# Performance work log

Hardware: AMD Instinct MI355X
Metric: run time of the kernel (lower is better)

## Reference

```python
import jax, jax.numpy as jnp
import numpy as np

M, IN, OUT = 8192, 4096, 4096
XOR_MASK = (1 << 3) | (1 << 7)  # 0x88: flips sign bit of each packed nibble


def _dequant_int4(weight_packed, weight_scales):
    """Decode packed int4 weights (offset-binary nibbles) to scaled float.

    weight_packed: [OUT, IN//2] int32, each byte holds two nibbles (v+8).
    Low nibble -> even input column, high nibble -> odd input column.
    """
    w = jnp.bitwise_xor(weight_packed, XOR_MASK)  # offset-binary -> two's complement nibbles
    low = jnp.bitwise_and(w, 0xF)
    high = jnp.bitwise_and(jnp.right_shift(w, 4), 0xF)
    low = jnp.where(low >= 8, low - 16, low)    # signed int4 in [-8, 7]
    high = jnp.where(high >= 8, high - 16, high)
    # interleave nibbles: [OUT, IN//2, 2] -> [OUT, IN]
    deq = jnp.stack([low, high], axis=-1).reshape(weight_packed.shape[0], -1)
    return deq.astype(weight_scales.dtype) * weight_scales[:, None]  # [OUT, IN]


def setup_inputs() -> dict:
    key = jax.random.key(0)
    k1, k2, k3, k4 = jax.random.split(key, 4)
    x = jax.random.normal(k1, (M, IN), dtype=jnp.float32)
    weight_packed = jax.random.randint(k2, (OUT, IN // 2), 0, 256, dtype=jnp.int32)
    weight_scales = jax.random.uniform(k3, (OUT,), dtype=jnp.float32) * 0.02 + 1e-3
    bias = jax.random.normal(k4, (OUT,), dtype=jnp.float32)
    return {"x": x, "weight_packed": weight_packed,
            "weight_scales": weight_scales, "bias": bias}


def reference(x, weight_packed, weight_scales, bias):
    # w4a16 forward: dequantize int4 weights per output row, then GEMM + bias.
    w = _dequant_int4(weight_packed, weight_scales)  # [OUT, IN]
    return jnp.dot(x, w.T) + bias  # [M, OUT]
```

## Files before the change

kernel.cpp:

```cpp
#include <hip/hip_runtime.h>
#include <cstdint>
#include <cstddef>

#define M_DIM 8192
#define K_DIM 4096
#define N_DIM 4096

typedef unsigned short u16;
typedef __bf16 bf16x8 __attribute__((ext_vector_type(8)));
typedef u16 u16x8 __attribute__((ext_vector_type(8)));
typedef float f32x4 __attribute__((ext_vector_type(4)));

__device__ __forceinline__ u16 f2bf_rne(float f) {
  uint32_t u = __builtin_bit_cast(uint32_t, f);
  return (u16)((u + 0x7FFFu + ((u >> 16) & 1u)) >> 16);
}
__device__ __forceinline__ u16 i2bf(int i) {
  return (u16)(__builtin_bit_cast(uint32_t, (float)i) >> 16);
}

#define XBLKS 16384
#define WBLKS 8192

__global__ __launch_bounds__(256) void prep(const float* __restrict__ x,
                                            const int* __restrict__ wp,
                                            u16* __restrict__ xb,
                                            u16* __restrict__ wb) {
  const int b = blockIdx.x;
  if (b < XBLKS) {
    size_t t = (size_t)b * 256 + threadIdx.x;
    const float4* xp = (const float4*)x;
    float4 a = xp[2 * t];
    float4 c = xp[2 * t + 1];
    u16x8 r;
    r[0] = f2bf_rne(a.x); r[1] = f2bf_rne(a.y); r[2] = f2bf_rne(a.z); r[3] = f2bf_rne(a.w);
    r[4] = f2bf_rne(c.x); r[5] = f2bf_rne(c.y); r[6] = f2bf_rne(c.z); r[7] = f2bf_rne(c.w);
    ((u16x8*)xb)[t] = r;
  } else {
    size_t t = (size_t)(b - XBLKS) * 256 + threadIdx.x;
    int4 p = ((const int4*)wp)[t];
    u16x8 r;
    int v;
    v = p.x ^ 0x88; r[0] = i2bf((v << 28) >> 28); r[1] = i2bf((v << 24) >> 28);
    v = p.y ^ 0x88; r[2] = i2bf((v << 28) >> 28); r[3] = i2bf((v << 24) >> 28);
    v = p.z ^ 0x88; r[4] = i2bf((v << 28) >> 28); r[5] = i2bf((v << 24) >> 28);
    v = p.w ^ 0x88; r[6] = i2bf((v << 28) >> 28); r[7] = i2bf((v << 24) >> 28);
    ((u16x8*)wb)[t] = r;
  }
}

__global__ __launch_bounds__(512, 2) void gemm_bt_w4a16(
    const u16* __restrict__ A,
    const u16* __restrict__ B,
    const float* __restrict__ scales,
    const float* __restrict__ bias,
    float* __restrict__ C) {
  __shared__ u16 sA[2][256 * 64];
  __shared__ u16 sB[2][256 * 64];

  const int tid = threadIdx.x;
  const int lane = tid & 63;
  const int wave = tid >> 6;
  const int m0 = blockIdx.y * 256;
  const int n0 = blockIdx.x * 256;
  const int wm = (wave >> 2) * 128;
  const int wn = (wave & 3) * 64;
  const int lrow = lane & 15;
  const int quad = lane >> 4;

  f32x4 acc[8][4] = {};

  const int srow = tid >> 3;
  const int schunk = ((tid & 7) ^ (srow & 7)) * 8;
  const u16* ga = A + (size_t)(m0 + srow) * K_DIM + schunk;
  const u16* gb = B + (size_t)(n0 + srow) * K_DIM + schunk;
  const int ldsoff = wave * 1024;

  auto stage = [&](int buf, int kb) {
#pragma unroll
    for (int r = 0; r < 4; ++r)
      __builtin_amdgcn_global_load_lds(
          (const __attribute__((address_space(1))) void*)(ga + (size_t)(r * 64) * K_DIM + kb),
          (__attribute__((address_space(3))) void*)((char*)sA[buf] + r * 8192 + ldsoff),
          16, 0, 0);
#pragma unroll
    for (int r = 0; r < 4; ++r)
      __builtin_amdgcn_global_load_lds(
          (const __attribute__((address_space(1))) void*)(gb + (size_t)(r * 64) * K_DIM + kb),
          (__attribute__((address_space(3))) void*)((char*)sB[buf] + r * 8192 + ldsoff),
          16, 0, 0);
  };

  auto compute = [&](int buf) {
    const u16* bA = sA[buf];
    const u16* bB = sB[buf];
#pragma unroll
    for (int s = 0; s < 2; ++s) {
      const int kc = ((s * 4 + quad) ^ (lrow & 7)) * 8;
      u16x8 af[8], bfr[4];
#pragma unroll
      for (int i = 0; i < 8; ++i)
        af[i] = *(const u16x8*)(bA + (wm + i * 16 + lrow) * 64 + kc);
#pragma unroll
      for (int j = 0; j < 4; ++j)
        bfr[j] = *(const u16x8*)(bB + (wn + j * 16 + lrow) * 64 + kc);
      __builtin_amdgcn_s_setprio(1);
#pragma unroll
      for (int i = 0; i < 8; ++i)
#pragma unroll
        for (int j = 0; j < 4; ++j)
          acc[i][j] = __builtin_amdgcn_mfma_f32_16x16x32_bf16(
              __builtin_bit_cast(bf16x8, af[i]),
              __builtin_bit_cast(bf16x8, bfr[j]), acc[i][j], 0, 0, 0);
      __builtin_amdgcn_s_setprio(0);
    }
  };

  stage(0, 0);
  __syncthreads();

#pragma unroll 1
  for (int it = 0; it < 32; ++it) {
    const int kb = it * 128;
    stage(1, kb + 64);
    compute(0);
    __syncthreads();
    if (it < 31) stage(0, kb + 128);
    compute(1);
    __syncthreads();
  }

#pragma unroll
  for (int j = 0; j < 4; ++j) {
    const int n = n0 + wn + j * 16 + lrow;
    const float sc = scales[n];
    const float bi = bias[n];
#pragma unroll
    for (int i = 0; i < 8; ++i) {
      const int m = m0 + wm + i * 16 + quad * 4;
      float* cp = &C[(size_t)m * N_DIM + n];
#pragma unroll
      for (int r = 0; r < 4; ++r)
        cp[(size_t)r * N_DIM] = acc[i][j][r] * sc + bi;
    }
  }
}

__global__ __launch_bounds__(256) void fallback_w4a16(
    const float* __restrict__ x, const int* __restrict__ wp,
    const float* __restrict__ scales, const float* __restrict__ bias,
    float* __restrict__ out) {
  const int n = blockIdx.x * 256 + threadIdx.x;
  const int m = blockIdx.y;
  const float* xr = x + (size_t)m * K_DIM;
  const int* wr = wp + (size_t)n * (K_DIM / 2);
  float acc = 0.f;
  for (int j = 0; j < K_DIM / 2; ++j) {
    int w = wr[j] ^ 0x88;
    float lo = (float)((w << 28) >> 28);
    float hi = (float)((w << 24) >> 28);
    acc += xr[2 * j] * lo + xr[2 * j + 1] * hi;
  }
  out[(size_t)m * N_DIM + n] = acc * scales[n] + bias[n];
}

extern "C" void kernel_launch(void* const* d_in, const int* in_sizes, int n_in,
                              void* d_out, int out_size, void* d_ws, size_t ws_size,
                              hipStream_t stream) {
  const float* x = (const float*)d_in[0];
  const int* wp = (const int*)d_in[1];
  const float* sc = (const float*)d_in[2];
  const float* bi = (const float*)d_in[3];
  float* out = (float*)d_out;

  const size_t xb_elems = (size_t)M_DIM * K_DIM;
  const size_t wb_elems = (size_t)N_DIM * K_DIM;
  const size_t need = (xb_elems + wb_elems) * sizeof(u16);

  if (ws_size >= need) {
    u16* xb = (u16*)d_ws;
    u16* wb = xb + xb_elems;
    prep<<<XBLKS + WBLKS, 256, 0, stream>>>(x, wp, xb, wb);
    gemm_bt_w4a16<<<dim3(N_DIM / 256, M_DIM / 256), 512, 0, stream>>>(xb, wb, sc, bi, out);
  } else {
    fallback_w4a16<<<dim3(N_DIM / 256, M_DIM), 256, 0, stream>>>(x, wp, sc, bi, out);
  }
}
```

Before: 476.2 us.

## Switch GEMM to 256x128 tiles with triple-buffered LDS pipeline and block swizzle

The bf16 GEMM tile shrinks from 256x256 to 256x128, so each of the eight waves now computes a 64x64 sub-tile. The LDS staging changes from a double buffer with two barriers per step to a three-stage ring that is prefetched two tiles ahead, using a single barrier and a partial vmcnt wait per K step. A 1D grid with an XOR-free block remap groups neighbouring tiles to improve L2 reuse. The aim is to hide global-load latency and cut barrier stalls, at the cost of lower arithmetic intensity per tile and more LDS per block.

```diff
diff --git a/kernel.cpp b/kernel.cpp
--- a/kernel.cpp
+++ b/kernel.cpp
@@ -5,6 +5,12 @@
 #define M_DIM 8192
 #define K_DIM 4096
 #define N_DIM 4096
+
+#define BM 256
+#define BN 128
+#define BK 64
+#define NBUF 3
+#define NT (K_DIM / BK)
 
 typedef unsigned short u16;
 typedef __bf16 bf16x8 __attribute__((ext_vector_type(8)));
@@ -55,20 +61,26 @@
     const float* __restrict__ scales,
     const float* __restrict__ bias,
     float* __restrict__ C) {
-  __shared__ u16 sA[2][256 * 64];
-  __shared__ u16 sB[2][256 * 64];
+  __shared__ u16 sA[NBUF][BM * BK];
+  __shared__ u16 sB[NBUF][BN * BK];
 
   const int tid = threadIdx.x;
   const int lane = tid & 63;
   const int wave = tid >> 6;
-  const int m0 = blockIdx.y * 256;
-  const int n0 = blockIdx.x * 256;
-  const int wm = (wave >> 2) * 128;
-  const int wn = (wave & 3) * 64;
+
+  const int flat = blockIdx.x;
+  const int swz = (flat & 7) * 128 + (flat >> 3);
+  const int bx = swz >> 5;
+  const int by = swz & 31;
+  const int m0 = by * BM;
+  const int n0 = bx * BN;
+
+  const int wm = (wave >> 1) * 64;
+  const int wn = (wave & 1) * 64;
   const int lrow = lane & 15;
   const int quad = lane >> 4;
 
-  f32x4 acc[8][4] = {};
+  f32x4 acc[4][4] = {};
 
   const int srow = tid >> 3;
   const int schunk = ((tid & 7) ^ (srow & 7)) * 8;
@@ -84,7 +96,7 @@
           (__attribute__((address_space(3))) void*)((char*)sA[buf] + r * 8192 + ldsoff),
           16, 0, 0);
 #pragma unroll
-    for (int r = 0; r < 4; ++r)
+    for (int r = 0; r < 2; ++r)
       __builtin_amdgcn_global_load_lds(
           (const __attribute__((address_space(1))) void*)(gb + (size_t)(r * 64) * K_DIM + kb),
           (__attribute__((address_space(3))) void*)((char*)sB[buf] + r * 8192 + ldsoff),
@@ -97,16 +109,16 @@
 #pragma unroll
     for (int s = 0; s < 2; ++s) {
       const int kc = ((s * 4 + quad) ^ (lrow & 7)) * 8;
-      u16x8 af[8], bfr[4];
-#pragma unroll
-      for (int i = 0; i < 8; ++i)
-        af[i] = *(const u16x8*)(bA + (wm + i * 16 + lrow) * 64 + kc);
+      u16x8 af[4], bfr[4];
+#pragma unroll
+      for (int i = 0; i < 4; ++i)
+        af[i] = *(const u16x8*)(bA + (wm + i * 16 + lrow) * BK + kc);
 #pragma unroll
       for (int j = 0; j < 4; ++j)
-        bfr[j] = *(const u16x8*)(bB + (wn + j * 16 + lrow) * 64 + kc);
+        bfr[j] = *(const u16x8*)(bB + (wn + j * 16 + lrow) * BK + kc);
       __builtin_amdgcn_s_setprio(1);
 #pragma unroll
-      for (int i = 0; i < 8; ++i)
+      for (int i = 0; i < 4; ++i)
 #pragma unroll
         for (int j = 0; j < 4; ++j)
           acc[i][j] = __builtin_amdgcn_mfma_f32_16x16x32_bf16(
@@ -117,18 +129,28 @@
   };
 
   stage(0, 0);
-  __syncthreads();
-
+  stage(1, BK);
+
+  int cur = 0;
 #pragma unroll 1
-  for (int it = 0; it < 32; ++it) {
-    const int kb = it * 128;
-    stage(1, kb + 64);
-    compute(0);
-    __syncthreads();
-    if (it < 31) stage(0, kb + 128);
-    compute(1);
-    __syncthreads();
-  }
+  for (int t = 0; t < NT - 1; ++t) {
+    asm volatile("s_waitcnt vmcnt(6)" ::: "memory");
+    __builtin_amdgcn_s_barrier();
+    __builtin_amdgcn_sched_barrier(0);
+
+    if (t + 2 < NT) {
+      int pre = cur + 2;
+      if (pre >= NBUF) pre -= NBUF;
+      stage(pre, (t + 2) * BK);
+    }
+    compute(cur);
+    cur = (cur == NBUF - 1) ? 0 : cur + 1;
+  }
+
+  asm volatile("s_waitcnt vmcnt(0)" ::: "memory");
+  __builtin_amdgcn_s_barrier();
+  __builtin_amdgcn_sched_barrier(0);
+  compute(cur);
 
 #pragma unroll
   for (int j = 0; j < 4; ++j) {
@@ -136,7 +158,7 @@
     const float sc = scales[n];
     const float bi = bias[n];
 #pragma unroll
-    for (int i = 0; i < 8; ++i) {
+    for (int i = 0; i < 4; ++i) {
       const int m = m0 + wm + i * 16 + quad * 4;
       float* cp = &C[(size_t)m * N_DIM + n];
 #pragma unroll
@@ -181,7 +203,7 @@
     u16* xb = (u16*)d_ws;
     u16* wb = xb + xb_elems;
     prep<<<XBLKS + WBLKS, 256, 0, stream>>>(x, wp, xb, wb);
-    gemm_bt_w4a16<<<dim3(N_DIM / 256, M_DIM / 256), 512, 0, stream>>>(xb, wb, sc, bi, out);
+    gemm_bt_w4a16<<<dim3((N_DIM / BN) * (M_DIM / BM)), 512, 0, stream>>>(xb, wb, sc, bi, out);
   } else {
     fallback_w4a16<<<dim3(N_DIM / 256, M_DIM), 256, 0, stream>>>(x, wp, sc, bi, out);
   }
```

New measurement: 615.1 us. 1.29x slower.

## Split LDS tiles into halves and interleave next-tile loads with MFMA

Applied to the files above, without the earlier changes.

Restructures the GEMM main loop so the A and B tiles are split into 128-row halves in separate LDS buffers, with the A0 half triple-buffered. Each iteration now needs only one barrier, gated by a manual vmcnt wait. The loads for the next K-tile are issued piecewise between MFMA groups, so memory traffic overlaps compute and fewer full-block syncs are needed. In exchange it depends on hand-tuned waitcnt counts and sched barriers, and uses more LDS (nine 16KB buffers), which can lower occupancy or introduce races if the counts are wrong.

```diff
diff --git a/kernel.cpp b/kernel.cpp
--- a/kernel.cpp
+++ b/kernel.cpp
@@ -5,6 +5,11 @@
 #define M_DIM 8192
 #define K_DIM 4096
 #define N_DIM 4096
+
+#define BM 256
+#define BN 256
+#define BK 64
+#define NT (K_DIM / BK)
 
 typedef unsigned short u16;
 typedef __bf16 bf16x8 __attribute__((ext_vector_type(8)));
@@ -55,18 +60,22 @@
     const float* __restrict__ scales,
     const float* __restrict__ bias,
     float* __restrict__ C) {
-  __shared__ u16 sA[2][256 * 64];
-  __shared__ u16 sB[2][256 * 64];
+  __shared__ u16 sA0[3][128 * 64];
+  __shared__ u16 sA1[2][128 * 64];
+  __shared__ u16 sB0[2][128 * 64];
+  __shared__ u16 sB1[2][128 * 64];
 
   const int tid = threadIdx.x;
   const int lane = tid & 63;
   const int wave = tid >> 6;
-  const int m0 = blockIdx.y * 256;
-  const int n0 = blockIdx.x * 256;
+  const int m0 = blockIdx.y * BM;
+  const int n0 = blockIdx.x * BN;
+
   const int wm = (wave >> 2) * 128;
   const int wn = (wave & 3) * 64;
   const int lrow = lane & 15;
   const int quad = lane >> 4;
+  const int brw0 = wn & 64;
 
   f32x4 acc[8][4] = {};
 
@@ -74,60 +83,91 @@
   const int schunk = ((tid & 7) ^ (srow & 7)) * 8;
   const u16* ga = A + (size_t)(m0 + srow) * K_DIM + schunk;
   const u16* gb = B + (size_t)(n0 + srow) * K_DIM + schunk;
-  const int ldsoff = wave * 1024;
-
-  auto stage = [&](int buf, int kb) {
-#pragma unroll
-    for (int r = 0; r < 4; ++r)
-      __builtin_amdgcn_global_load_lds(
-          (const __attribute__((address_space(1))) void*)(ga + (size_t)(r * 64) * K_DIM + kb),
-          (__attribute__((address_space(3))) void*)((char*)sA[buf] + r * 8192 + ldsoff),
-          16, 0, 0);
-#pragma unroll
-    for (int r = 0; r < 4; ++r)
-      __builtin_amdgcn_global_load_lds(
-          (const __attribute__((address_space(1))) void*)(gb + (size_t)(r * 64) * K_DIM + kb),
-          (__attribute__((address_space(3))) void*)((char*)sB[buf] + r * 8192 + ldsoff),
-          16, 0, 0);
-  };
-
-  auto compute = [&](int buf) {
-    const u16* bA = sA[buf];
-    const u16* bB = sB[buf];
+  const int dst0 = tid * 16;
+
+#define GLDS(gp, lp)                                                      \
+  __builtin_amdgcn_global_load_lds(                                       \
+      (const __attribute__((address_space(1))) void*)(gp),                \
+      (__attribute__((address_space(3))) void*)(lp), 16, 0, 0)
+
+  auto stA0 = [&](int slot, int T) {
+    const u16* g = ga + (size_t)T * BK;
+    char* d = (char*)sA0[slot] + dst0;
+    GLDS(g, d);
+    GLDS(g + (size_t)64 * K_DIM, d + 8192);
+  };
+  auto stA1 = [&](int b, int T) {
+    const u16* g = ga + (size_t)128 * K_DIM + (size_t)T * BK;
+    char* d = (char*)sA1[b] + dst0;
+    GLDS(g, d);
+    GLDS(g + (size_t)64 * K_DIM, d + 8192);
+  };
+  auto stB0 = [&](int b, int T) {
+    const u16* g = gb + (size_t)T * BK;
+    char* d = (char*)sB0[b] + dst0;
+    GLDS(g, d);
+    GLDS(g + (size_t)64 * K_DIM, d + 8192);
+  };
+  auto stB1 = [&](int b, int T) {
+    const u16* g = gb + (size_t)128 * K_DIM + (size_t)T * BK;
+    char* d = (char*)sB1[b] + dst0;
+    GLDS(g, d);
+    GLDS(g + (size_t)64 * K_DIM, d + 8192);
+  };
+
+  stA0(0, 0); stA1(0, 0); stB0(0, 0); stB1(0, 0);
+
+  int a0slot = 0;
+#pragma unroll 1
+  for (int T = 0; T < NT; ++T) {
+    const int buf = T & 1;
+    const int nbuf = buf ^ 1;
+    const bool more = (T + 1 < NT);
+    int a0next = a0slot + 1; if (a0next == 3) a0next = 0;
+
+    if (more) {
+      stA0(a0next, T + 1);
+      asm volatile("s_waitcnt vmcnt(2)" ::: "memory");
+    } else {
+      asm volatile("s_waitcnt vmcnt(0)" ::: "memory");
+    }
+    __builtin_amdgcn_s_barrier();
+    __builtin_amdgcn_sched_barrier(0);
+
+    const u16* aH = (wave < 4) ? sA0[a0slot] : sA1[buf];
+    const u16* bH = (wn < 128) ? sB0[buf] : sB1[buf];
+
 #pragma unroll
     for (int s = 0; s < 2; ++s) {
       const int kc = ((s * 4 + quad) ^ (lrow & 7)) * 8;
-      u16x8 af[8], bfr[4];
-#pragma unroll
-      for (int i = 0; i < 8; ++i)
-        af[i] = *(const u16x8*)(bA + (wm + i * 16 + lrow) * 64 + kc);
+      u16x8 bfr[4];
 #pragma unroll
       for (int j = 0; j < 4; ++j)
-        bfr[j] = *(const u16x8*)(bB + (wn + j * 16 + lrow) * 64 + kc);
-      __builtin_amdgcn_s_setprio(1);
-#pragma unroll
-      for (int i = 0; i < 8; ++i)
-#pragma unroll
-        for (int j = 0; j < 4; ++j)
-          acc[i][j] = __builtin_amdgcn_mfma_f32_16x16x32_bf16(
-              __builtin_bit_cast(bf16x8, af[i]),
-              __builtin_bit_cast(bf16x8, bfr[j]), acc[i][j], 0, 0, 0);
-      __builtin_amdgcn_s_setprio(0);
+        bfr[j] = *(const u16x8*)(bH + (brw0 + j * 16 + lrow) * BK + kc);
+#pragma unroll
+      for (int ih = 0; ih < 2; ++ih) {
+        u16x8 af[4];
+#pragma unroll
+        for (int i = 0; i < 4; ++i)
+          af[i] = *(const u16x8*)(aH + (ih * 64 + i * 16 + lrow) * BK + kc);
+        if (more) {
+          if (s == 0 && ih == 0) stA1(nbuf, T + 1);
+          if (s == 0 && ih == 1) stB0(nbuf, T + 1);
+          if (s == 1 && ih == 0) stB1(nbuf, T + 1);
+        }
+        __builtin_amdgcn_s_setprio(1);
+#pragma unroll
+        for (int i = 0; i < 4; ++i)
+#pragma unroll
+          for (int j = 0; j < 4; ++j)
+            acc[ih * 4 + i][j] = __builtin_amdgcn_mfma_f32_16x16x32_bf16(
+                __builtin_bit_cast(bf16x8, af[i]),
+                __builtin_bit_cast(bf16x8, bfr[j]), acc[ih * 4 + i][j], 0, 0, 0);
+        __builtin_amdgcn_s_setprio(0);
+        __builtin_amdgcn_sched_barrier(0);
+      }
     }
-  };
-
-  stage(0, 0);
-  __syncthreads();
-
-#pragma unroll 1
-  for (int it = 0; it < 32; ++it) {
-    const int kb = it * 128;
-    stage(1, kb + 64);
-    compute(0);
-    __syncthreads();
-    if (it < 31) stage(0, kb + 128);
-    compute(1);
-    __syncthreads();
+    a0slot = a0next;
   }
 
 #pragma unroll
@@ -144,6 +184,7 @@
         cp[(size_t)r * N_DIM] = acc[i][j][r] * sc + bi;
     }
   }
+#undef GLDS
 }
 
 __global__ __launch_bounds__(256) void fallback_w4a16(
@@ -181,7 +222,7 @@
     u16* xb = (u16*)d_ws;
     u16* wb = xb + xb_elems;
     prep<<<XBLKS + WBLKS, 256, 0, stream>>>(x, wp, xb, wb);
-    gemm_bt_w4a16<<<dim3(N_DIM / 256, M_DIM / 256), 512, 0, stream>>>(xb, wb, sc, bi, out);
+    gemm_bt_w4a16<<<dim3(N_DIM / BN, M_DIM / BM), 512, 0, stream>>>(xb, wb, sc, bi, out);
   } else {
     fallback_w4a16<<<dim3(N_DIM / 256, M_DIM), 256, 0, stream>>>(x, wp, sc, bi, out);
   }
```

Result: no change. 469.7 us (-1.4%).
